# Kernel tuning notes

Hardware: AMD Instinct MI355X
Metric: run time of the kernel (lower is better)

The kernel has to match this reference:

```python
import jax, jax.numpy as jnp
import numpy as np

EMB = 256
N_NODES = 100000
N_EDGES = 500000
N_REL = 10
REL_DIM = 64
HID = 128
HEADS = 4
HEAD_DIM = HID // HEADS


def setup_inputs() -> dict:
    key = jax.random.key(0)
    ks = jax.random.split(key, 16)
    s = lambda i, shape: jax.random.normal(ks[i], shape, dtype=jnp.float32) * 0.05
    return {
        "node_embeddings": jax.random.normal(ks[0], (N_NODES, EMB), dtype=jnp.float32),
        "edge_index": jax.random.randint(ks[1], (2, N_EDGES), 0, N_NODES),
        "relation_type": jax.random.randint(ks[2], (N_EDGES,), 0, N_REL),
        "rel_emb": s(3, (N_REL, REL_DIM)),
        "W_edge": s(4, (2 * EMB, HID)), "b_edge": jnp.zeros((HID,), jnp.float32),
        "W_q": s(5, (REL_DIM, HID)), "b_q": jnp.zeros((HID,), jnp.float32),
        "W_k": s(6, (HID, HID)), "b_k": jnp.zeros((HID,), jnp.float32),
        "W_v": s(7, (HID, HID)), "b_v": jnp.zeros((HID,), jnp.float32),
        "W_o1": s(8, (HID, HID)), "b_o1": jnp.zeros((HID,), jnp.float32),
        "W_o2": s(9, (HID, 1)), "b_o2": jnp.zeros((1,), jnp.float32),
    }


def reference(node_embeddings, edge_index, relation_type, rel_emb,
              W_edge, b_edge, W_q, b_q, W_k, b_k, W_v, b_v,
              W_o1, b_o1, W_o2, b_o2):
    # Gather endpoint features: [E, 2*EMB]
    src = node_embeddings[edge_index[0]]
    tgt = node_embeddings[edge_index[1]]
    edge_features = jnp.concatenate([src, tgt], axis=1)
    # Edge MLP (dropout is identity at eval): [E, HID]
    edge_hidden = jax.nn.relu(edge_features @ W_edge + b_edge)
    # Relation embedding lookup: [E, REL_DIM]
    rel = rel_emb[relation_type]
    E = edge_hidden.shape[0]
    Q = (rel @ W_q + b_q).reshape(E, HEADS, HEAD_DIM)
    K = (edge_hidden @ W_k + b_k).reshape(E, HEADS, HEAD_DIM)
    V = (edge_hidden @ W_v + b_v).reshape(E, HEADS, HEAD_DIM)
    scale = jnp.sqrt(jnp.float32(HEAD_DIM))
    scores = jnp.sum(Q * K, axis=-1) / scale          # [E, HEADS]
    attn = jax.nn.softmax(scores, axis=-1)            # softmax over heads
    attended = (attn[..., None] * V).reshape(E, HID)
    output = attended + edge_hidden
    # Output MLP: Linear->ReLU->Linear(1)
    h = jax.nn.relu(output @ W_o1 + b_o1)
    score = (h @ W_o2 + b_o2).squeeze(-1)             # [E]
    return score
```

## Files before the change

### kernel.cpp

```cpp
#include <hip/hip_runtime.h>

#define EMB   256
#define HID   128
#define RELD  64
#define NREL  10
#define TE    64

typedef __attribute__((ext_vector_type(8)))  short bf16x8;
typedef __attribute__((ext_vector_type(16))) float f32x16;

__device__ __forceinline__ float bf16_to_f32(unsigned short u) {
    union { unsigned int i; float f; } v;
    v.i = ((unsigned int)u) << 16;
    return v.f;
}

__device__ __forceinline__ unsigned short f32_to_bf16(float x) {
    union { unsigned int i; float f; } v;
    v.f = x;
    unsigned int b = v.i;
    unsigned int rounded = b + 0x7fffu + ((b >> 16) & 1u);
    return (unsigned short)(rounded >> 16);
}

template <bool F32>
__device__ __forceinline__ float ldx(const void* p, size_t i) {
    if (F32) return ((const float*)p)[i];
    return bf16_to_f32(((const unsigned short*)p)[i]);
}

__device__ __forceinline__ bool detect_f32(const void* nodeEmb) {
    const float* f = (const float*)nodeEmb;
    float x = f[(threadIdx.x & 63) * 997];
    bool sane = isfinite(x) && fabsf(x) < 1.0e6f;
    unsigned long long m = __ballot(sane);
    return __popcll(m) >= 48;
}

template <bool F32>
__device__ void prep_body(int vb, const void* W_edge, const void* W_k,
                          const void* W_v, const void* W_o1, const void* rel_emb,
                          const void* W_q, const void* b_q,
                          unsigned short* WTe, unsigned short* WTk,
                          unsigned short* WTv, unsigned short* WTo1, float* Qtab)
{
    if (vb < 448) {
        int idx = vb * 256 + threadIdx.x;
        if (idx < 65536) {
            int kc = idx >> 12, e = idx & 4095;
            int g = e >> 3, j = e & 7;
            int col = g & 127, kg = g >> 7;
            int k = kc * 32 + kg * 8 + j;
            WTe[idx] = f32_to_bf16(ldx<F32>(W_edge, (size_t)k * HID + col));
        } else if (idx < 65536 + 16384) {
            int i = idx - 65536;
            int kc = i >> 12, e = i & 4095;
            int g = e >> 3, j = e & 7;
            int col = g & 127, kg = (g >> 7) & 3;
            int k = kc * 32 + kg * 8 + j;
            WTk[i] = f32_to_bf16(ldx<F32>(W_k, (size_t)k * HID + col));
        } else if (idx < 65536 + 2 * 16384) {
            int i = idx - 65536 - 16384;
            int kc = i >> 12, e = i & 4095;
            int g = e >> 3, j = e & 7;
            int col = g & 127, kg = (g >> 7) & 3;
            int k = kc * 32 + kg * 8 + j;
            WTv[i] = f32_to_bf16(ldx<F32>(W_v, (size_t)k * HID + col));
        } else {
            int i = idx - 65536 - 2 * 16384;
            int kc = i >> 12, e = i & 4095;
            int g = e >> 3, j = e & 7;
            int col = g & 127, kg = (g >> 7) & 3;
            int k = kc * 32 + kg * 8 + j;
            WTo1[i] = f32_to_bf16(ldx<F32>(W_o1, (size_t)k * HID + col));
        }
    } else {
        const int t = threadIdx.x;
        const int c = t & (HID - 1);
        const int h = t >> 7;
        for (int r = h; r < NREL; r += 2) {
            float acc = 0.f;
            for (int d = 0; d < RELD; ++d)
                acc += ldx<F32>(rel_emb, r * RELD + d) * ldx<F32>(W_q, (size_t)d * HID + c);
            Qtab[r * HID + c] = acc + ldx<F32>(b_q, c);
        }
    }
}

__global__ void prep_kernel(const void* nodeEmb,
                            const void* W_edge, const void* W_k, const void* W_v,
                            const void* W_o1, const void* rel_emb, const void* W_q,
                            const void* b_q,
                            unsigned short* WTe, unsigned short* WTk,
                            unsigned short* WTv, unsigned short* WTo1, float* Qtab,
                            unsigned short* nodeBf16, int convBlocks,
                            unsigned long long nodeElems)
{
    bool f32 = detect_f32(nodeEmb);
    int b = blockIdx.x;
    if (b < convBlocks) {
        if (!f32) return;
        unsigned long long i = (unsigned long long)b * 2048ull + threadIdx.x * 8;
        if (i + 8 <= nodeElems) {
            const float* src = (const float*)nodeEmb + i;
            float4 f0 = *(const float4*)src;
            float4 f1 = *(const float4*)(src + 4);
            union { unsigned short us[8]; uint4 v; } pk;
            pk.us[0] = f32_to_bf16(f0.x); pk.us[1] = f32_to_bf16(f0.y);
            pk.us[2] = f32_to_bf16(f0.z); pk.us[3] = f32_to_bf16(f0.w);
            pk.us[4] = f32_to_bf16(f1.x); pk.us[5] = f32_to_bf16(f1.y);
            pk.us[6] = f32_to_bf16(f1.z); pk.us[7] = f32_to_bf16(f1.w);
            *(uint4*)(nodeBf16 + i) = pk.v;
        }
        return;
    }
    b -= convBlocks;
    if (f32) prep_body<true >(b, W_edge, W_k, W_v, W_o1, rel_emb, W_q, b_q,
                              WTe, WTk, WTv, WTo1, Qtab);
    else     prep_body<false>(b, W_edge, W_k, W_v, W_o1, rel_emb, W_q, b_q,
                              WTe, WTk, WTv, WTo1, Qtab);
}

struct __align__(16) Smem {
    unsigned short sHid[TE][136];
    union {
        unsigned short sA[TE][40];
        float sQf[NREL * HID];
    } u;
    unsigned short sB[4096];
    float sBias[5 * HID];
    float sSc[TE][4], sAttn[TE][4];
    float sPart[TE][2];
    int   sSrc[TE], sTgt[TE], sRel[TE];
};

__device__ __forceinline__ void gemm128(Smem& sm, const unsigned short* WT,
                                        f32x16* acc, int t, int rt, int cg2,
                                        int c, int h5)
{
    for (int kc = 0; kc < 4; ++kc) {
        const unsigned short* base = WT + kc * 4096;
        __syncthreads();
        *(uint4*)&sm.sB[(size_t)t * 8]         = *(const uint4*)(base + (size_t)t * 8);
        *(uint4*)&sm.sB[(size_t)(t + 256) * 8] = *(const uint4*)(base + (size_t)(t + 256) * 8);
        __syncthreads();
        #pragma unroll
        for (int s = 0; s < 2; ++s) {
            bf16x8 a = *(const bf16x8*)&sm.sHid[32 * rt + c][kc * 32 + s * 16 + h5 * 8];
            #pragma unroll
            for (int ct = 0; ct < 2; ++ct) {
                bf16x8 b = *(const bf16x8*)
                    &sm.sB[((s * 2 + h5) * 128 + 64 * cg2 + 32 * ct + c) * 8];
                acc[ct] = __builtin_amdgcn_mfma_f32_32x32x16_bf16(a, b, acc[ct], 0, 0, 0);
            }
        }
    }
}

template <bool F32, bool GBF16>
__device__ void fused_body(
    Smem& sm,
    const void* gsrc, const int* edgeIdx, const int* relType,
    const unsigned short* WTe, const unsigned short* WTk,
    const unsigned short* WTv, const unsigned short* WTo1,
    const void* b_edge, const void* b_k, const void* b_v,
    const void* b_o1, const void* W_o2, const void* b_o2,
    const float* Qtab, void* outp, int E)
{
    const int t   = threadIdx.x;
    const int l   = t & 63;
    const int w   = t >> 6;
    const int c   = l & 31;
    const int h5  = l >> 5;
    const int rt  = w & 1;
    const int cg2 = w >> 1;
    const int bs  = blockIdx.x * TE;

    if (t < TE) {
        int e = bs + t;
        if (e >= E) e = E - 1;
        if (e < 0)  e = 0;
        sm.sSrc[t] = edgeIdx[e];
        sm.sTgt[t] = edgeIdx[E + e];
        int r = relType[e];
        if (r < 0) r = 0;
        if (r >= NREL) r = NREL - 1;
        sm.sRel[t] = r;
    }
    for (int i = t; i < 5 * HID; i += 256) {
        int which = i >> 7, j = i & (HID - 1);
        float v = (which == 0) ? ldx<F32>(b_edge, j)
                : (which == 1) ? ldx<F32>(b_k, j)
                : (which == 2) ? ldx<F32>(b_v, j)
                : (which == 3) ? ldx<F32>(b_o1, j)
                               : ldx<F32>(W_o2, j);
        sm.sBias[i] = v;
    }
    __syncthreads();

    const int edge_s = t >> 2;
    const int grp    = t & 3;

    f32x16 acc[2];
    acc[0] = (f32x16)(0.0f); acc[1] = (f32x16)(0.0f);
    for (int kc = 0; kc < 16; ++kc) {
        __syncthreads();
        {
            int node = (kc < 8) ? sm.sSrc[edge_s] : sm.sTgt[edge_s];
            int col0 = (kc & 7) * 32 + grp * 8;
            if (GBF16) {
                *(uint4*)&sm.u.sA[edge_s][grp * 8] =
                    *(const uint4*)((const unsigned short*)gsrc +
                                    (size_t)node * EMB + col0);
            } else {
                const float* p = (const float*)gsrc + (size_t)node * EMB + col0;
                float4 f0 = *(const float4*)p;
                float4 f1 = *(const float4*)(p + 4);
                union { unsigned short us[8]; uint4 v; } pk;
                pk.us[0] = f32_to_bf16(f0.x); pk.us[1] = f32_to_bf16(f0.y);
                pk.us[2] = f32_to_bf16(f0.z); pk.us[3] = f32_to_bf16(f0.w);
                pk.us[4] = f32_to_bf16(f1.x); pk.us[5] = f32_to_bf16(f1.y);
                pk.us[6] = f32_to_bf16(f1.z); pk.us[7] = f32_to_bf16(f1.w);
                *(uint4*)&sm.u.sA[edge_s][grp * 8] = pk.v;
            }
        }
        {
            const unsigned short* base = WTe + kc * 4096;
            *(uint4*)&sm.sB[(size_t)t * 8]         = *(const uint4*)(base + (size_t)t * 8);
            *(uint4*)&sm.sB[(size_t)(t + 256) * 8] = *(const uint4*)(base + (size_t)(t + 256) * 8);
        }
        __syncthreads();
        #pragma unroll
        for (int s = 0; s < 2; ++s) {
            bf16x8 a = *(const bf16x8*)&sm.u.sA[32 * rt + c][s * 16 + h5 * 8];
            #pragma unroll
            for (int ct = 0; ct < 2; ++ct) {
                bf16x8 b = *(const bf16x8*)
                    &sm.sB[((s * 2 + h5) * 128 + 64 * cg2 + 32 * ct + c) * 8];
                acc[ct] = __builtin_amdgcn_mfma_f32_32x32x16_bf16(a, b, acc[ct], 0, 0, 0);
            }
        }
    }
    {
        #pragma unroll
        for (int ct = 0; ct < 2; ++ct) {
            int col = 64 * cg2 + 32 * ct + c;
            float bb = sm.sBias[col];
            #pragma unroll
            for (int r = 0; r < 16; ++r) {
                int erow = 32 * rt + (r & 3) + 8 * (r >> 2) + 4 * h5;
                sm.sHid[erow][col] = f32_to_bf16(fmaxf(acc[ct][r] + bb, 0.f));
            }
        }
    }
    __syncthreads();
    for (int i = t; i < NREL * HID; i += 256)
        sm.u.sQf[i] = Qtab[i];

    f32x16 kacc[2];
    kacc[0] = (f32x16)(0.0f); kacc[1] = (f32x16)(0.0f);
    gemm128(sm, WTk, kacc, t, rt, cg2, c, h5);

    {
        float ps[2][16];
        #pragma unroll
        for (int ct = 0; ct < 2; ++ct) {
            int col = 64 * cg2 + 32 * ct + c;
            float bk = sm.sBias[HID + col];
            #pragma unroll
            for (int r = 0; r < 16; ++r) {
                int erow = 32 * rt + (r & 3) + 8 * (r >> 2) + 4 * h5;
                ps[ct][r] = (kacc[ct][r] + bk) * sm.u.sQf[sm.sRel[erow] * HID + col];
            }
        }
        #pragma unroll
        for (int m = 1; m < 32; m <<= 1)
            #pragma unroll
            for (int ct = 0; ct < 2; ++ct)
                #pragma unroll
                for (int r = 0; r < 16; ++r)
                    ps[ct][r] += __shfl_xor(ps[ct][r], m, 64);
        if (c == 0) {
            const float inv = 0.17677669529663687f;
            #pragma unroll
            for (int ct = 0; ct < 2; ++ct) {
                int head = 2 * cg2 + ct;
                #pragma unroll
                for (int r = 0; r < 16; ++r) {
                    int erow = 32 * rt + (r & 3) + 8 * (r >> 2) + 4 * h5;
                    sm.sSc[erow][head] = ps[ct][r] * inv;
                }
            }
        }
    }
    __syncthreads();
    if (t < TE) {
        float s0 = sm.sSc[t][0], s1 = sm.sSc[t][1];
        float s2 = sm.sSc[t][2], s3 = sm.sSc[t][3];
        float m = fmaxf(fmaxf(s0, s1), fmaxf(s2, s3));
        float e0 = expf(s0 - m), e1 = expf(s1 - m);
        float e2 = expf(s2 - m), e3 = expf(s3 - m);
        float den = e0 + e1 + e2 + e3;
        sm.sAttn[t][0] = e0 / den; sm.sAttn[t][1] = e1 / den;
        sm.sAttn[t][2] = e2 / den; sm.sAttn[t][3] = e3 / den;
    }
    __syncthreads();

    f32x16 vacc[2];
    vacc[0] = (f32x16)(0.0f); vacc[1] = (f32x16)(0.0f);
    gemm128(sm, WTv, vacc, t, rt, cg2, c, h5);
    {
        #pragma unroll
        for (int ct = 0; ct < 2; ++ct) {
            int col  = 64 * cg2 + 32 * ct + c;
            int head = 2 * cg2 + ct;
            float bv = sm.sBias[2 * HID + col];
            #pragma unroll
            for (int r = 0; r < 16; ++r) {
                int erow = 32 * rt + (r & 3) + 8 * (r >> 2) + 4 * h5;
                float at = sm.sAttn[erow][head];
                float hv = bf16_to_f32(sm.sHid[erow][col]);
                sm.sHid[erow][col] = f32_to_bf16(at * (vacc[ct][r] + bv) + hv);
            }
        }
    }

    f32x16 oacc[2];
    oacc[0] = (f32x16)(0.0f); oacc[1] = (f32x16)(0.0f);
    gemm128(sm, WTo1, oacc, t, rt, cg2, c, h5);
    {
        float pr[16];
        #pragma unroll
        for (int r = 0; r < 16; ++r) pr[r] = 0.f;
        #pragma unroll
        for (int ct = 0; ct < 2; ++ct) {
            int col = 64 * cg2 + 32 * ct + c;
            float bo = sm.sBias[3 * HID + col];
            float wo = sm.sBias[4 * HID + col];
            #pragma unroll
            for (int r = 0; r < 16; ++r)
                pr[r] += fmaxf(oacc[ct][r] + bo, 0.f) * wo;
        }
        #pragma unroll
        for (int m = 1; m < 32; m <<= 1)
            #pragma unroll
            for (int r = 0; r < 16; ++r)
                pr[r] += __shfl_xor(pr[r], m, 64);
        if (c == 0) {
            #pragma unroll
            for (int r = 0; r < 16; ++r) {
                int erow = 32 * rt + (r & 3) + 8 * (r >> 2) + 4 * h5;
                sm.sPart[erow][cg2] = pr[r];
            }
        }
    }
    __syncthreads();
    if (t < TE) {
        int ge = bs + t;
        if (ge < E) {
            float val = sm.sPart[t][0] + sm.sPart[t][1] + ldx<F32>(b_o2, 0);
            if (F32) ((float*)outp)[ge] = val;
            else     ((unsigned short*)outp)[ge] = f32_to_bf16(val);
        }
    }
}

__global__ __launch_bounds__(256, 4) void RelationAttentionMLPHead_10539849744626_kernel(
    const void* nodeEmb, const unsigned short* nodeBf16, int useConv,
    const int* edgeIdx, const int* relType,
    const unsigned short* WTe, const unsigned short* WTk,
    const unsigned short* WTv, const unsigned short* WTo1,
    const void* b_edge, const void* b_k, const void* b_v,
    const void* b_o1, const void* W_o2, const void* b_o2,
    const float* Qtab, void* outp, int E)
{
    __shared__ Smem sm;
    if (detect_f32(nodeEmb)) {
        if (useConv)
            fused_body<true, true >(sm, nodeBf16, edgeIdx, relType, WTe, WTk, WTv, WTo1,
                                    b_edge, b_k, b_v, b_o1, W_o2, b_o2, Qtab, outp, E);
        else
            fused_body<true, false>(sm, nodeEmb, edgeIdx, relType, WTe, WTk, WTv, WTo1,
                                    b_edge, b_k, b_v, b_o1, W_o2, b_o2, Qtab, outp, E);
    } else {
        fused_body<false, true>(sm, nodeEmb, edgeIdx, relType, WTe, WTk, WTv, WTo1,
                                b_edge, b_k, b_v, b_o1, W_o2, b_o2, Qtab, outp, E);
    }
}

extern "C" void kernel_launch(void* const* d_in, const int* in_sizes, int n_in,
                              void* d_out, int out_size, void* d_ws, size_t ws_size,
                              hipStream_t stream) {
    (void)n_in;

    const void* nodeEmb = d_in[0];
    const int*  edgeIdx = (const int*)d_in[1];
    const int*  relType = (const int*)d_in[2];
    const void* rel_emb = d_in[3];
    const void* W_edge  = d_in[4];
    const void* b_edge  = d_in[5];
    const void* W_q     = d_in[6];
    const void* b_q     = d_in[7];
    const void* W_k     = d_in[8];
    const void* b_k     = d_in[9];
    const void* W_v     = d_in[10];
    const void* b_v     = d_in[11];
    const void* W_o1    = d_in[12];
    const void* b_o1    = d_in[13];
    const void* W_o2    = d_in[14];
    const void* b_o2    = d_in[15];

    int E = out_size;
    if (E <= 0) E = in_sizes ? in_sizes[2] : 0;
    if (E <= 0) E = 500000;

    unsigned long long nodeElems =
        (in_sizes && in_sizes[0] > 0) ? (unsigned long long)in_sizes[0] : 25600000ull;

    char* ws = (char*)d_ws;
    float*          Qtab     = (float*)ws;
    unsigned short* WTe      = (unsigned short*)(ws + 8192);
    unsigned short* WTk      = (unsigned short*)(ws + 139264);
    unsigned short* WTv      = (unsigned short*)(ws + 172032);
    unsigned short* WTo1     = (unsigned short*)(ws + 204800);
    unsigned short* nodeBf16 = (unsigned short*)(ws + 237568);

    size_t need = 237568ull + nodeElems * 2ull;
    int useConv = (ws_size >= need) ? 1 : 0;
    int convBlocks = useConv ? (int)((nodeElems + 2047ull) / 2048ull) : 0;

    prep_kernel<<<convBlocks + 449, 256, 0, stream>>>(
        nodeEmb, W_edge, W_k, W_v, W_o1, rel_emb, W_q, b_q,
        WTe, WTk, WTv, WTo1, Qtab, nodeBf16, convBlocks, nodeElems);

    int grid = (E + TE - 1) / TE;
    if (grid < 1) grid = 1;

    RelationAttentionMLPHead_10539849744626_kernel<<<grid, 256, 0, stream>>>(
        nodeEmb, nodeBf16, useConv, edgeIdx, relType, WTe, WTk, WTv, WTo1,
        b_edge, b_k, b_v, b_o1, W_o2, b_o2, Qtab, d_out, E);
}
```

Measured before the change: 443.8 us.

## Double-buffer LDS tiles and prefetch next K-chunk into registers

Both the edge GEMM (gathered node rows plus W_edge tiles) and the 128x128 GEMMs now keep two LDS buffers. The next chunk is loaded into registers before the MFMAs of the current chunk and written to the other buffer afterwards, so each iteration needs one barrier instead of two and global latency can overlap compute. Shared memory and register use grow, so launch bounds are relaxed from 4 to 3 blocks per CU, which may reduce occupancy for this gather-bound kernel.

New measurement: 461.7 us. 1.04x slower.

```diff
diff --git a/kernel.cpp b/kernel.cpp
--- a/kernel.cpp
+++ b/kernel.cpp
@@ -124,10 +124,10 @@
 struct __align__(16) Smem {
     unsigned short sHid[TE][136];
     union {
-        unsigned short sA[TE][40];
+        unsigned short sA[2][TE][40];
         float sQf[NREL * HID];
     } u;
-    unsigned short sB[4096];
+    unsigned short sB[2][4096];
     float sBias[5 * HID];
     float sSc[TE][4], sAttn[TE][4];
     float sPart[TE][2];
@@ -138,22 +138,36 @@
                                         f32x16* acc, int t, int rt, int cg2,
                                         int c, int h5)
 {
+    {
+        uint4 b0 = *(const uint4*)(WT + (size_t)t * 8);
+        uint4 b1 = *(const uint4*)(WT + (size_t)(t + 256) * 8);
+        *(uint4*)&sm.sB[0][(size_t)t * 8]         = b0;
+        *(uint4*)&sm.sB[0][(size_t)(t + 256) * 8] = b1;
+    }
+    __syncthreads();
     for (int kc = 0; kc < 4; ++kc) {
-        const unsigned short* base = WT + kc * 4096;
-        __syncthreads();
-        *(uint4*)&sm.sB[(size_t)t * 8]         = *(const uint4*)(base + (size_t)t * 8);
-        *(uint4*)&sm.sB[(size_t)(t + 256) * 8] = *(const uint4*)(base + (size_t)(t + 256) * 8);
-        __syncthreads();
+        const int bi = kc & 1;
+        uint4 n0, n1;
+        if (kc < 3) {
+            const unsigned short* nb = WT + (size_t)(kc + 1) * 4096;
+            n0 = *(const uint4*)(nb + (size_t)t * 8);
+            n1 = *(const uint4*)(nb + (size_t)(t + 256) * 8);
+        }
         #pragma unroll
         for (int s = 0; s < 2; ++s) {
             bf16x8 a = *(const bf16x8*)&sm.sHid[32 * rt + c][kc * 32 + s * 16 + h5 * 8];
             #pragma unroll
             for (int ct = 0; ct < 2; ++ct) {
                 bf16x8 b = *(const bf16x8*)
-                    &sm.sB[((s * 2 + h5) * 128 + 64 * cg2 + 32 * ct + c) * 8];
+                    &sm.sB[bi][((s * 2 + h5) * 128 + 64 * cg2 + 32 * ct + c) * 8];
                 acc[ct] = __builtin_amdgcn_mfma_f32_32x32x16_bf16(a, b, acc[ct], 0, 0, 0);
             }
         }
+        if (kc < 3) {
+            *(uint4*)&sm.sB[bi ^ 1][(size_t)t * 8]         = n0;
+            *(uint4*)&sm.sB[bi ^ 1][(size_t)(t + 256) * 8] = n1;
+        }
+        __syncthreads();
     }
 }
 
@@ -203,43 +217,74 @@
 
     f32x16 acc[2];
     acc[0] = (f32x16)(0.0f); acc[1] = (f32x16)(0.0f);
+    {
+        int node = sm.sSrc[edge_s];
+        if (GBF16) {
+            uint4 pa = *(const uint4*)((const unsigned short*)gsrc +
+                                       (size_t)node * EMB + grp * 8);
+            *(uint4*)&sm.u.sA[0][edge_s][grp * 8] = pa;
+        } else {
+            const float* p = (const float*)gsrc + (size_t)node * EMB + grp * 8;
+            float4 f0 = *(const float4*)p;
+            float4 f1 = *(const float4*)(p + 4);
+            union { unsigned short us[8]; uint4 v; } pk;
+            pk.us[0] = f32_to_bf16(f0.x); pk.us[1] = f32_to_bf16(f0.y);
+            pk.us[2] = f32_to_bf16(f0.z); pk.us[3] = f32_to_bf16(f0.w);
+            pk.us[4] = f32_to_bf16(f1.x); pk.us[5] = f32_to_bf16(f1.y);
+            pk.us[6] = f32_to_bf16(f1.z); pk.us[7] = f32_to_bf16(f1.w);
+            *(uint4*)&sm.u.sA[0][edge_s][grp * 8] = pk.v;
+        }
+        uint4 b0 = *(const uint4*)(WTe + (size_t)t * 8);
+        uint4 b1 = *(const uint4*)(WTe + (size_t)(t + 256) * 8);
+        *(uint4*)&sm.sB[0][(size_t)t * 8]         = b0;
+        *(uint4*)&sm.sB[0][(size_t)(t + 256) * 8] = b1;
+    }
+    __syncthreads();
     for (int kc = 0; kc < 16; ++kc) {
-        __syncthreads();
-        {
-            int node = (kc < 8) ? sm.sSrc[edge_s] : sm.sTgt[edge_s];
-            int col0 = (kc & 7) * 32 + grp * 8;
+        const int bi = kc & 1;
+        uint4 pa, pb0, pb1;
+        float4 f0, f1;
+        if (kc < 15) {
+            int kn = kc + 1;
+            int node = (kn < 8) ? sm.sSrc[edge_s] : sm.sTgt[edge_s];
+            int col0 = (kn & 7) * 32 + grp * 8;
             if (GBF16) {
-                *(uint4*)&sm.u.sA[edge_s][grp * 8] =
-                    *(const uint4*)((const unsigned short*)gsrc +
-                                    (size_t)node * EMB + col0);
+                pa = *(const uint4*)((const unsigned short*)gsrc +
+                                     (size_t)node * EMB + col0);
             } else {
                 const float* p = (const float*)gsrc + (size_t)node * EMB + col0;
-                float4 f0 = *(const float4*)p;
-                float4 f1 = *(const float4*)(p + 4);
+                f0 = *(const float4*)p;
+                f1 = *(const float4*)(p + 4);
+            }
+            const unsigned short* nb = WTe + (size_t)kn * 4096;
+            pb0 = *(const uint4*)(nb + (size_t)t * 8);
+            pb1 = *(const uint4*)(nb + (size_t)(t + 256) * 8);
+        }
+        #pragma unroll
+        for (int s = 0; s < 2; ++s) {
+            bf16x8 a = *(const bf16x8*)&sm.u.sA[bi][32 * rt + c][s * 16 + h5 * 8];
+            #pragma unroll
+            for (int ct = 0; ct < 2; ++ct) {
+                bf16x8 b = *(const bf16x8*)
+                    &sm.sB[bi][((s * 2 + h5) * 128 + 64 * cg2 + 32 * ct + c) * 8];
+                acc[ct] = __builtin_amdgcn_mfma_f32_32x32x16_bf16(a, b, acc[ct], 0, 0, 0);
+            }
+        }
+        if (kc < 15) {
+            if (GBF16) {
+                *(uint4*)&sm.u.sA[bi ^ 1][edge_s][grp * 8] = pa;
+            } else {
                 union { unsigned short us[8]; uint4 v; } pk;
                 pk.us[0] = f32_to_bf16(f0.x); pk.us[1] = f32_to_bf16(f0.y);
                 pk.us[2] = f32_to_bf16(f0.z); pk.us[3] = f32_to_bf16(f0.w);
                 pk.us[4] = f32_to_bf16(f1.x); pk.us[5] = f32_to_bf16(f1.y);
                 pk.us[6] = f32_to_bf16(f1.z); pk.us[7] = f32_to_bf16(f1.w);
-                *(uint4*)&sm.u.sA[edge_s][grp * 8] = pk.v;
-            }
-        }
-        {
-            const unsigned short* base = WTe + kc * 4096;
-            *(uint4*)&sm.sB[(size_t)t * 8]         = *(const uint4*)(base + (size_t)t * 8);
-            *(uint4*)&sm.sB[(size_t)(t + 256) * 8] = *(const uint4*)(base + (size_t)(t + 256) * 8);
+                *(uint4*)&sm.u.sA[bi ^ 1][edge_s][grp * 8] = pk.v;
+            }
+            *(uint4*)&sm.sB[bi ^ 1][(size_t)t * 8]         = pb0;
+            *(uint4*)&sm.sB[bi ^ 1][(size_t)(t + 256) * 8] = pb1;
         }
         __syncthreads();
-        #pragma unroll
-        for (int s = 0; s < 2; ++s) {
-            bf16x8 a = *(const bf16x8*)&sm.u.sA[32 * rt + c][s * 16 + h5 * 8];
-            #pragma unroll
-            for (int ct = 0; ct < 2; ++ct) {
-                bf16x8 b = *(const bf16x8*)
-                    &sm.sB[((s * 2 + h5) * 128 + 64 * cg2 + 32 * ct + c) * 8];
-                acc[ct] = __builtin_amdgcn_mfma_f32_32x32x16_bf16(a, b, acc[ct], 0, 0, 0);
-            }
-        }
     }
     {
         #pragma unroll
@@ -365,7 +410,7 @@
     }
 }
 
-__global__ __launch_bounds__(256, 4) void RelationAttentionMLPHead_10539849744626_kernel(
+__global__ __launch_bounds__(256, 3) void RelationAttentionMLPHead_10539849744626_kernel(
     const void* nodeEmb, const unsigned short* nodeBf16, int useConv,
     const int* edgeIdx, const int* relType,
     const unsigned short* WTe, const unsigned short* WTk,
```
